# Performance work log

Hardware: AMD Instinct MI355X
Metric: run time of the kernel (lower is better)

The kernel has to match this reference:

```python
import jax, jax.numpy as jnp
import numpy as np

H_HEADS = 4

def setup_inputs() -> dict:
    key = jax.random.key(0)
    ks = jax.random.split(key, 14)
    B, C, H, W = 8, 512, 32, 32
    r = C // H_HEADS  # SE reduction = h per SelfModule(channel, h)
    s_in = 0.02
    inp = {
        'x': jax.random.normal(ks[0], (B, C, H, W), jnp.float32),
        'wq': jax.random.normal(ks[1], (C, C), jnp.float32) * s_in,
        'bq': jnp.zeros((C,), jnp.float32),
        'wk': jax.random.normal(ks[2], (C, C), jnp.float32) * s_in,
        'bk': jnp.zeros((C,), jnp.float32),
        'wv': jax.random.normal(ks[3], (C, C), jnp.float32) * s_in,
        'bv': jnp.zeros((C,), jnp.float32),
        'fc1_w': jax.random.normal(ks[4], (r, C), jnp.float32) * s_in,
        'fc1_b': jnp.zeros((r,), jnp.float32),
        'fc2_w': jax.random.normal(ks[5], (C, r), jnp.float32) * s_in,
        'fc2_b': jnp.zeros((C,), jnp.float32),
        'gate_w': jax.random.normal(ks[6], (1, C), jnp.float32) * s_in,
        'gate_b': jnp.zeros((1,), jnp.float32),
    }
    return inp

def _conv1x1(y, w, b):
    # y: [B,C,H,W], w: [O,C] (1x1 conv kernel squeezed), b: [O]
    return jnp.einsum('bchw,oc->bohw', y, w) + b[None, :, None, None]

def reference(x, wq, bq, wk, bk, wv, bv, fc1_w, fc1_b, fc2_w, fc2_b, gate_w, gate_b):
    B, C, H, W = x.shape
    h = H_HEADS
    dk = C // h
    N = H * W

    # --- SelfScaling (SE without final sigmoid-in-block; sigmoid applied at mul) ---
    p = x.mean(axis=(2, 3))                                   # [B,C] global avg pool
    f = jax.nn.relu(p @ fc1_w.T + fc1_b) @ fc2_w.T + fc2_b    # [B,C]
    x = x * jax.nn.sigmoid(f)[:, :, None, None] + x

    # --- RTrans: conv1x1 QKV, attention over flattened H*W ---
    q = _conv1x1(x, wq, bq).reshape(B, h, dk, N).transpose(0, 1, 3, 2)  # [B,h,N,dk]
    k = _conv1x1(x, wk, bk).reshape(B, h, dk, N)                        # [B,h,dk,N]
    v = _conv1x1(x, wv, bv).reshape(B, h, dk, N)                        # [B,h,dk,N]
    scale = 1.0 / float(np.sqrt(dk))
    att = jax.nn.softmax(jnp.einsum('bhnd,bhdm->bhnm', q, k) * scale, axis=-1)  # [B,h,N,N]
    o = jnp.einsum('bhdn,bhnm->bhdm', v, att).reshape(B, C, H, W)  # v @ att as in torch

    # --- SelfGating ---
    gate = jax.nn.sigmoid(_conv1x1(o, gate_w, gate_b))  # [B,1,H,W]
    return o * gate + o
```

## Files before the change

### kernel.cpp

```cpp
#include <hip/hip_runtime.h>
#include <hip/hip_bf16.h>

#define B_ 8
#define C_ 512
#define N_ 1024
#define HEADS_ 4
#define DK_ 128
#define R_ 128

typedef float f32x4 __attribute__((ext_vector_type(4)));
typedef __bf16 bf16x8 __attribute__((ext_vector_type(8)));
typedef short short4v __attribute__((ext_vector_type(4)));
typedef unsigned short u16;

constexpr float kScale = 0.08838834764831845f;

#define OFF_P   0u
#define OFF_SS  16384u
#define OFF_WB  32768u
#define OFF_XT  1605632u
#define OFF_QT  9994240u
#define OFF_KT  18382848u
#define OFF_V   26771456u
#define OFF_DEN 35160064u
#define OFF_G   35291136u

__device__ __forceinline__ u16 f2b(float f) {
  __hip_bfloat16 h = __float2bfloat16(f);
  return __builtin_bit_cast(u16, h);
}

typedef const __attribute__((address_space(1))) unsigned int* gptr_t;
typedef __attribute__((address_space(3))) unsigned int* lptr_t;
__device__ __forceinline__ void gload16(const void* g, void* l) {
  __builtin_amdgcn_global_load_lds((gptr_t)g, (lptr_t)l, 16, 0, 0);
}

__device__ __forceinline__ f32x4 mfma16(bf16x8 a, bf16x8 b, f32x4 c) {
  return __builtin_amdgcn_mfma_f32_16x16x32_bf16(a, b, c, 0, 0, 0);
}

#if __has_builtin(__builtin_amdgcn_mfma_f32_16x16x16bf16_1k)
__device__ __forceinline__ f32x4 mfma_k16(short4v a, short4v b, f32x4 c) {
  return __builtin_amdgcn_mfma_f32_16x16x16bf16_1k(a, b, c, 0, 0, 0);
}
#else
__device__ __forceinline__ f32x4 mfma_k16(short4v a, short4v b, f32x4 c) {
  bf16x8 a8 = {}, b8 = {};
  for (int e = 0; e < 4; e++) {
    ((u16*)&a8)[e] = ((u16*)&a)[e];
    ((u16*)&b8)[e] = ((u16*)&b)[e];
  }
  return __builtin_amdgcn_mfma_f32_16x16x32_bf16(a8, b8, c, 0, 0, 0);
}
#endif

__global__ __launch_bounds__(64) void k_pool(const float* __restrict__ x,
                                             float* __restrict__ p) {
  int bc = blockIdx.x, lane = threadIdx.x;
  const float4* row = (const float4*)(x + (size_t)bc * N_);
  float s = 0.f;
  for (int i = lane; i < N_ / 4; i += 64) {
    float4 t = row[i];
    s += t.x + t.y + t.z + t.w;
  }
  for (int o = 32; o > 0; o >>= 1) s += __shfl_down(s, o, 64);
  if (lane == 0) p[bc] = s * (1.0f / N_);
}

__global__ __launch_bounds__(256) void k_se(const float* __restrict__ p,
                                            const float* __restrict__ fc1w,
                                            const float* __restrict__ fc1b,
                                            const float* __restrict__ fc2w,
                                            const float* __restrict__ fc2b,
                                            float* __restrict__ ss) {
  __shared__ float pl[C_];
  __shared__ float f1[R_];
  int b = blockIdx.x, t = threadIdx.x;
  for (int c = t; c < C_; c += 256) pl[c] = p[b * C_ + c];
  __syncthreads();
  if (t < R_) {
    float a = fc1b[t];
    for (int c = 0; c < C_; c++) a += pl[c] * fc1w[t * C_ + c];
    f1[t] = fmaxf(a, 0.f);
  }
  __syncthreads();
  for (int c = t; c < C_; c += 256) {
    float a = fc2b[c];
    for (int j = 0; j < R_; j++) a += f1[j] * fc2w[c * R_ + j];
    ss[b * C_ + c] = 1.f + 1.f / (1.f + __expf(-a));
  }
}

__global__ __launch_bounds__(256) void k_castw(const float* __restrict__ wq,
                                               const float* __restrict__ wk,
                                               const float* __restrict__ wv,
                                               u16* __restrict__ wb) {
  int i = blockIdx.x * 256 + threadIdx.x;
  int idx = i * 4;
  const float* srcs[3] = {wq, wk, wv};
  int w = idx / (C_ * C_), off = idx % (C_ * C_);
  float4 v = *(const float4*)(srcs[w] + off);
  u16* d = wb + idx;
  d[0] = f2b(v.x); d[1] = f2b(v.y); d[2] = f2b(v.z); d[3] = f2b(v.w);
}

__global__ __launch_bounds__(256) void k_xt(const float* __restrict__ x,
                                            const float* __restrict__ ss,
                                            u16* __restrict__ xt) {
  int b = blockIdx.z, c0 = blockIdx.y * 64, n0 = blockIdx.x * 64;
  __shared__ float tile[64][65];
  int t = threadIdx.x;
  int cr = t >> 4, nc4 = (t & 15) * 4;
  for (int j = 0; j < 4; j++) {
    int c = cr + j * 16;
    float sc = ss[b * C_ + c0 + c];
    float4 v = *(const float4*)(x + ((size_t)b * C_ + c0 + c) * N_ + n0 + nc4);
    tile[c][nc4 + 0] = v.x * sc;
    tile[c][nc4 + 1] = v.y * sc;
    tile[c][nc4 + 2] = v.z * sc;
    tile[c][nc4 + 3] = v.w * sc;
  }
  __syncthreads();
  int nr = t >> 2, cc = (t & 3) * 16;
  u16 ov[16];
  for (int m = 0; m < 16; m++) ov[m] = f2b(tile[cc + m][nr]);
  u16* dst = xt + ((size_t)b * N_ + n0 + nr) * C_ + c0 + cc;
  for (int m = 0; m < 16; m++) dst[m] = ov[m];
}

__global__ __launch_bounds__(256) void k_qkv(const u16* __restrict__ xt,
                                             const u16* __restrict__ wb,
                                             const float* __restrict__ bq,
                                             const float* __restrict__ bk,
                                             const float* __restrict__ bv,
                                             u16* __restrict__ qt,
                                             u16* __restrict__ kt,
                                             u16* __restrict__ v) {
  __shared__ char smem[32768];
  int b = blockIdx.y / 3, sel = blockIdx.y % 3;
  int tile = blockIdx.x;
  const char *Ab, *Bb;
  u16* out;
  const float* bias;
  int mt, nt, rstride;
  size_t xtoff = (size_t)b * N_ * C_;
  if (sel < 2) {
    mt = tile & 7; nt = tile >> 3;
    Ab = (const char*)(xt + xtoff + (size_t)mt * 128 * C_);
    Bb = (const char*)(wb + (size_t)sel * C_ * C_ + (size_t)nt * 128 * C_);
    out = (sel ? kt : qt) + xtoff;
    bias = sel ? bk : bq;
    rstride = C_ * 2;
  } else {
    mt = tile & 3; nt = tile >> 2;
    Ab = (const char*)(wb + (size_t)2 * C_ * C_ + (size_t)mt * 128 * C_);
    Bb = (const char*)(xt + xtoff + (size_t)nt * 128 * C_);
    out = v + (size_t)b * C_ * N_;
    bias = bv;
    rstride = N_ * 2;
  }
  int t = threadIdx.x, lane = t & 63, wid = t >> 6;
  int wr = wid >> 1, wc = wid & 1;
  const f32x4 z4 = {0.f, 0.f, 0.f, 0.f};
  f32x4 acc[4][4];
  for (int i = 0; i < 4; i++)
    for (int j = 0; j < 4; j++) acc[i][j] = z4;

  char* lA = smem;
  char* lB = smem + 16384;
  for (int ko = 0; ko < C_; ko += 64) {
    __syncthreads();
    for (int i = wid; i < 16; i += 4) {
      int beta = i * 1024 + lane * 16;
      int row = beta >> 7, cb = (beta & 127) ^ ((row & 7) << 4);
      gload16(Ab + (size_t)row * 1024 + ko * 2 + cb, lA + beta);
    }
    for (int i = wid; i < 16; i += 4) {
      int beta = i * 1024 + lane * 16;
      int row = beta >> 7, cb = (beta & 127) ^ ((row & 7) << 4);
      gload16(Bb + (size_t)row * 1024 + ko * 2 + cb, lB + beta);
    }
    __syncthreads();
    for (int ks = 0; ks < 2; ks++) {
      int kb = ks * 64 + (lane >> 4) * 16;
      bf16x8 af[4], bfr[4];
      for (int fi = 0; fi < 4; fi++) {
        int row = wr * 64 + fi * 16 + (lane & 15);
        af[fi] = *(const bf16x8*)(lA + row * 128 + (kb ^ ((row & 7) << 4)));
      }
      for (int fj = 0; fj < 4; fj++) {
        int row = wc * 64 + fj * 16 + (lane & 15);
        bfr[fj] = *(const bf16x8*)(lB + row * 128 + (kb ^ ((row & 7) << 4)));
      }
      for (int fi = 0; fi < 4; fi++)
        for (int fj = 0; fj < 4; fj++)
          acc[fi][fj] = mfma16(af[fi], bfr[fj], acc[fi][fj]);
    }
  }
  __syncthreads();
  for (int fi = 0; fi < 4; fi++)
    for (int fj = 0; fj < 4; fj++) {
      int colb = wc * 64 + fj * 16 + (lane & 15);
      for (int r = 0; r < 4; r++) {
        int rowb = wr * 64 + fi * 16 + (lane >> 4) * 4 + r;
        float bva = (sel < 2) ? bias[nt * 128 + colb] : bias[mt * 128 + rowb];
        float val = acc[fi][fj][r] + bva;
        int byte = rowb * 256 + ((colb * 2) ^ ((rowb & 7) << 4));
        *(u16*)(smem + byte) = f2b(val);
      }
    }
  __syncthreads();
  for (int i = t; i < 2048; i += 256) {
    int row = i >> 4, cb = (i & 15) * 16;
    bf16x8 val = *(const bf16x8*)(smem + row * 256 + (cb ^ ((row & 7) << 4)));
    *(bf16x8*)((char*)out + (size_t)(mt * 128 + row) * rstride + nt * 256 + cb) = val;
  }
}

__global__ __launch_bounds__(256) void k_passA(const u16* __restrict__ qt,
                                               const u16* __restrict__ kt,
                                               float* __restrict__ invden) {
  __shared__ char lK[2][32768];
  int bh = blockIdx.x, nb = blockIdx.y * 128;
  int b = bh >> 2, h = bh & 3;
  const char* qb = (const char*)(qt + (size_t)b * N_ * C_ + h * DK_);
  const char* kb = (const char*)(kt + (size_t)b * N_ * C_ + h * DK_);
  int t = threadIdx.x, lane = t & 63, wid = t >> 6;
  bf16x8 aq[2][4];
  for (int gq = 0; gq < 2; gq++) {
    const char* qr = qb + (size_t)(nb + wid * 32 + gq * 16 + (lane & 15)) * (C_ * 2);
    for (int ks = 0; ks < 4; ks++)
      aq[gq][ks] = *(const bf16x8*)(qr + ks * 64 + (lane >> 4) * 16);
  }
  float sacc[2][4] = {{0.f, 0.f, 0.f, 0.f}, {0.f, 0.f, 0.f, 0.f}};
  const f32x4 z4 = {0.f, 0.f, 0.f, 0.f};
  for (int i = wid; i < 32; i += 4) {
    int beta = i * 1024 + lane * 16;
    int row = beta >> 8, cb = (beta & 255) ^ ((row & 7) << 4);
    gload16(kb + (size_t)row * (C_ * 2) + cb, lK[0] + beta);
  }
  for (int mc = 0; mc < 8; mc++) {
    int cur = mc & 1;
    __syncthreads();
    if (mc < 7) {
      int mnext = (mc + 1) * 128;
      for (int i = wid; i < 32; i += 4) {
        int beta = i * 1024 + lane * 16;
        int row = beta >> 8, cb = (beta & 255) ^ ((row & 7) << 4);
        gload16(kb + (size_t)(mnext + row) * (C_ * 2) + cb, lK[cur ^ 1] + beta);
      }
    }
    for (int fj = 0; fj < 8; fj++) {
      f32x4 s0 = z4, s1 = z4;
      for (int ks = 0; ks < 4; ks++) {
        int row = fj * 16 + (lane & 15);
        bf16x8 bk_ = *(const bf16x8*)(lK[cur] + row * 256 +
                                      ((ks * 64 + (lane >> 4) * 16) ^ ((row & 7) << 4)));
        s0 = mfma16(aq[0][ks], bk_, s0);
        s1 = mfma16(aq[1][ks], bk_, s1);
      }
      for (int r = 0; r < 4; r++) {
        sacc[0][r] += __expf(s0[r] * kScale);
        sacc[1][r] += __expf(s1[r] * kScale);
      }
    }
  }
  for (int gq = 0; gq < 2; gq++)
    for (int r = 0; r < 4; r++) {
      float vv = sacc[gq][r];
      for (int m = 1; m < 16; m <<= 1) vv += __shfl_xor(vv, m, 64);
      sacc[gq][r] = vv;
    }
  if ((lane & 15) == 0) {
    for (int gq = 0; gq < 2; gq++) {
      int n = nb + wid * 32 + gq * 16 + (lane >> 4) * 4;
      for (int r = 0; r < 4; r++) invden[(size_t)bh * N_ + n + r] = 1.f / sacc[gq][r];
    }
  }
}

__global__ __launch_bounds__(256) void k_passB(const u16* __restrict__ qt,
                                               const u16* __restrict__ kt,
                                               const u16* __restrict__ v,
                                               const float* __restrict__ invden,
                                               const float* __restrict__ gw,
                                               float* __restrict__ out,
                                               float* __restrict__ g) {
  __shared__ char lQ[2][16384];
  __shared__ char lV[2][16384];
  __shared__ float gacc[128];
  int bh = blockIdx.x, mb = blockIdx.y * 128;
  int b = bh >> 2, h = bh & 3;
  const char* qb = (const char*)(qt + (size_t)b * N_ * C_ + h * DK_);
  const char* kb = (const char*)(kt + (size_t)b * N_ * C_ + h * DK_);
  const char* vb = (const char*)(v + ((size_t)b * C_ + h * DK_) * N_);
  float* ob = out + ((size_t)b * C_ + h * DK_) * N_ + mb;
  const float* idenb = invden + (size_t)bh * N_;
  int t = threadIdx.x, lane = t & 63, wid = t >> 6;
  bf16x8 bkm[2][4];
  for (int gi = 0; gi < 2; gi++) {
    const char* kr = kb + (size_t)(mb + wid * 32 + gi * 16 + (lane & 15)) * (C_ * 2);
    for (int ks = 0; ks < 4; ks++)
      bkm[gi][ks] = *(const bf16x8*)(kr + ks * 64 + (lane >> 4) * 16);
  }
  if (t < 128) gacc[t] = 0.f;
  const f32x4 z4 = {0.f, 0.f, 0.f, 0.f};
  f32x4 oacc[2][8];
  for (int gi = 0; gi < 2; gi++)
    for (int j = 0; j < 8; j++) oacc[gi][j] = z4;

  for (int i = wid; i < 16; i += 4) {
    int beta = i * 1024 + lane * 16;
    int row = beta >> 8, cb = (beta & 255) ^ ((row & 7) << 4);
    gload16(qb + (size_t)row * (C_ * 2) + cb, lQ[0] + beta);
  }
  for (int i = wid; i < 16; i += 4) {
    int beta = i * 1024 + lane * 16;
    int row = beta >> 7, cb = (beta & 127) ^ ((row & 7) << 4);
    gload16(vb + (size_t)row * (N_ * 2) + cb, lV[0] + beta);
  }

  for (int nc = 0; nc < 16; nc++) {
    int n0 = nc * 64, cur = nc & 1;
    __syncthreads();
    if (nc < 15) {
      int nn = n0 + 64;
      for (int i = wid; i < 16; i += 4) {
        int beta = i * 1024 + lane * 16;
        int row = beta >> 8, cb = (beta & 255) ^ ((row & 7) << 4);
        gload16(qb + (size_t)(nn + row) * (C_ * 2) + cb, lQ[cur ^ 1] + beta);
      }
      for (int i = wid; i < 16; i += 4) {
        int beta = i * 1024 + lane * 16;
        int row = beta >> 7, cb = (beta & 127) ^ ((row & 7) << 4);
        gload16(vb + (size_t)row * (N_ * 2) + nn * 2 + cb, lV[cur ^ 1] + beta);
      }
    }
    short4v pf[2][4];
    for (int fj = 0; fj < 4; fj++) {
      f32x4 s0 = z4, s1 = z4;
      for (int ks = 0; ks < 4; ks++) {
        int row = fj * 16 + (lane & 15);
        bf16x8 aq = *(const bf16x8*)(lQ[cur] + row * 256 +
                                     ((ks * 64 + (lane >> 4) * 16) ^ ((row & 7) << 4)));
        s0 = mfma16(aq, bkm[0][ks], s0);
        s1 = mfma16(aq, bkm[1][ks], s1);
      }
      float4 id4 = *(const float4*)(idenb + n0 + fj * 16 + (lane >> 4) * 4);
      short4v p0, p1;
      p0[0] = (short)f2b(__expf(s0[0] * kScale) * id4.x);
      p0[1] = (short)f2b(__expf(s0[1] * kScale) * id4.y);
      p0[2] = (short)f2b(__expf(s0[2] * kScale) * id4.z);
      p0[3] = (short)f2b(__expf(s0[3] * kScale) * id4.w);
      p1[0] = (short)f2b(__expf(s1[0] * kScale) * id4.x);
      p1[1] = (short)f2b(__expf(s1[1] * kScale) * id4.y);
      p1[2] = (short)f2b(__expf(s1[2] * kScale) * id4.z);
      p1[3] = (short)f2b(__expf(s1[3] * kScale) * id4.w);
      pf[0][fj] = p0;
      pf[1][fj] = p1;
    }
    for (int fd = 0; fd < 8; fd++) {
      int row = fd * 16 + (lane & 15);
      const char* vr = lV[cur] + row * 128;
      int sw = (row & 7) << 4;
      for (int fj = 0; fj < 4; fj++) {
        short4v av = *(const short4v*)(vr + ((fj * 32 + (lane >> 4) * 8) ^ sw));
        oacc[0][fd] = mfma_k16(av, pf[0][fj], oacc[0][fd]);
        oacc[1][fd] = mfma_k16(av, pf[1][fj], oacc[1][fd]);
      }
    }
  }
  __syncthreads();
  for (int gi = 0; gi < 2; gi++) {
    float part = 0.f;
    int mcol = wid * 32 + gi * 16 + (lane & 15);
    for (int fd = 0; fd < 8; fd++) {
      float4 gwv = *(const float4*)(gw + h * DK_ + fd * 16 + (lane >> 4) * 4);
      float gwa[4] = {gwv.x, gwv.y, gwv.z, gwv.w};
      for (int r = 0; r < 4; r++) {
        float val = oacc[gi][fd][r];
        int d = fd * 16 + (lane >> 4) * 4 + r;
        ob[(size_t)d * N_ + mcol] = val;
        part += gwa[r] * val;
      }
    }
    atomicAdd(&gacc[mcol], part);
  }
  __syncthreads();
  if (t < 128) atomicAdd(&g[(size_t)b * N_ + mb + t], gacc[t]);
}

__global__ __launch_bounds__(256) void k_zero_g(float* __restrict__ g) {
  g[blockIdx.x * 256 + threadIdx.x] = 0.f;
}

__global__ __launch_bounds__(256) void k_gate_apply(const float* __restrict__ g,
                                                    const float* __restrict__ gb,
                                                    float* __restrict__ out) {
  size_t i = ((size_t)blockIdx.x * 256 + threadIdx.x) * 4;
  int b = (int)(i / ((size_t)C_ * N_));
  int n = (int)(i & (N_ - 1));
  float4 gv = *(const float4*)(g + (size_t)b * N_ + n);
  float bias = gb[0];
  float4 v = *(float4*)(out + i);
  v.x *= 1.f + 1.f / (1.f + __expf(-(gv.x + bias)));
  v.y *= 1.f + 1.f / (1.f + __expf(-(gv.y + bias)));
  v.z *= 1.f + 1.f / (1.f + __expf(-(gv.z + bias)));
  v.w *= 1.f + 1.f / (1.f + __expf(-(gv.w + bias)));
  *(float4*)(out + i) = v;
}

extern "C" void kernel_launch(void* const* d_in, const int* in_sizes, int n_in,
                              void* d_out, int out_size, void* d_ws, size_t ws_size,
                              hipStream_t stream) {
  const float* x    = (const float*)d_in[0];
  const float* wq   = (const float*)d_in[1];
  const float* bq   = (const float*)d_in[2];
  const float* wk   = (const float*)d_in[3];
  const float* bk   = (const float*)d_in[4];
  const float* wv   = (const float*)d_in[5];
  const float* bv   = (const float*)d_in[6];
  const float* fc1w = (const float*)d_in[7];
  const float* fc1b = (const float*)d_in[8];
  const float* fc2w = (const float*)d_in[9];
  const float* fc2b = (const float*)d_in[10];
  const float* gw   = (const float*)d_in[11];
  const float* gb   = (const float*)d_in[12];
  float* out = (float*)d_out;
  char* ws = (char*)d_ws;

  float* p   = (float*)(ws + OFF_P);
  float* ssc = (float*)(ws + OFF_SS);
  u16* wb  = (u16*)(ws + OFF_WB);
  u16* xt  = (u16*)(ws + OFF_XT);
  u16* qt  = (u16*)(ws + OFF_QT);
  u16* kt  = (u16*)(ws + OFF_KT);
  u16* v   = (u16*)(ws + OFF_V);
  float* den = (float*)(ws + OFF_DEN);
  float* g   = (float*)(ws + OFF_G);

  k_pool<<<B_ * C_, 64, 0, stream>>>(x, p);
  k_castw<<<768, 256, 0, stream>>>(wq, wk, wv, wb);
  k_se<<<B_, 256, 0, stream>>>(p, fc1w, fc1b, fc2w, fc2b, ssc);
  k_zero_g<<<B_ * N_ / 256, 256, 0, stream>>>(g);
  k_xt<<<dim3(16, 8, B_), 256, 0, stream>>>(x, ssc, xt);
  k_qkv<<<dim3(32, B_ * 3), 256, 0, stream>>>(xt, wb, bq, bk, bv, qt, kt, v);
  k_passA<<<dim3(32, 8), 256, 0, stream>>>(qt, kt, den);
  k_passB<<<dim3(32, 8), 256, 0, stream>>>(qt, kt, v, den, gw, out, g);
  k_gate_apply<<<B_ * C_ * N_ / 1024, 256, 0, stream>>>(g, gb, out);
}
```

Before: 127.8 us.

## Split attention passes over key/query halves to double grid parallelism

Pass A now splits the key range into two halves across a new grid dimension and atomically accumulates the softmax denominators, which are zeroed in a merged cast/zero kernel. Pass B splits the query (reduction) dimension into two halves. One half writes to the output and the other to a workspace buffer, and the gate kernel sums the two partial results. This doubles the grid from 256 to 512 blocks so more CUs are used, at the cost of an extra 16MB partial buffer to write and read, atomics, and a per-element reciprocal in pass B. The separate zero kernel launch is also folded into the cast kernel.

```diff
diff --git a/kernel.cpp b/kernel.cpp
--- a/kernel.cpp
+++ b/kernel.cpp
@@ -24,6 +24,7 @@
 #define OFF_V   26771456u
 #define OFF_DEN 35160064u
 #define OFF_G   35291136u
+#define OFF_O1  35323904u
 
 __device__ __forceinline__ u16 f2b(float f) {
   __hip_bfloat16 h = __float2bfloat16(f);
@@ -92,11 +93,22 @@
   }
 }
 
-__global__ __launch_bounds__(256) void k_castw(const float* __restrict__ wq,
-                                               const float* __restrict__ wk,
-                                               const float* __restrict__ wv,
-                                               u16* __restrict__ wb) {
-  int i = blockIdx.x * 256 + threadIdx.x;
+__global__ __launch_bounds__(256) void k_castw_zero(const float* __restrict__ wq,
+                                                    const float* __restrict__ wk,
+                                                    const float* __restrict__ wv,
+                                                    u16* __restrict__ wb,
+                                                    float* __restrict__ g,
+                                                    float* __restrict__ den) {
+  int bid = blockIdx.x;
+  if (bid >= 800) {
+    den[(bid - 800) * 256 + threadIdx.x] = 0.f;
+    return;
+  }
+  if (bid >= 768) {
+    g[(bid - 768) * 256 + threadIdx.x] = 0.f;
+    return;
+  }
+  int i = bid * 256 + threadIdx.x;
   int idx = i * 4;
   const float* srcs[3] = {wq, wk, wv};
   int w = idx / (C_ * C_), off = idx % (C_ * C_);
@@ -220,9 +232,9 @@
 
 __global__ __launch_bounds__(256) void k_passA(const u16* __restrict__ qt,
                                                const u16* __restrict__ kt,
-                                               float* __restrict__ invden) {
+                                               float* __restrict__ den) {
   __shared__ char lK[2][32768];
-  int bh = blockIdx.x, nb = blockIdx.y * 128;
+  int bh = blockIdx.x, nb = blockIdx.y * 128, mh = blockIdx.z;
   int b = bh >> 2, h = bh & 3;
   const char* qb = (const char*)(qt + (size_t)b * N_ * C_ + h * DK_);
   const char* kb = (const char*)(kt + (size_t)b * N_ * C_ + h * DK_);
@@ -235,16 +247,17 @@
   }
   float sacc[2][4] = {{0.f, 0.f, 0.f, 0.f}, {0.f, 0.f, 0.f, 0.f}};
   const f32x4 z4 = {0.f, 0.f, 0.f, 0.f};
+  int m0 = mh * 512;
   for (int i = wid; i < 32; i += 4) {
     int beta = i * 1024 + lane * 16;
     int row = beta >> 8, cb = (beta & 255) ^ ((row & 7) << 4);
-    gload16(kb + (size_t)row * (C_ * 2) + cb, lK[0] + beta);
-  }
-  for (int mc = 0; mc < 8; mc++) {
+    gload16(kb + (size_t)(m0 + row) * (C_ * 2) + cb, lK[0] + beta);
+  }
+  for (int mc = 0; mc < 4; mc++) {
     int cur = mc & 1;
     __syncthreads();
-    if (mc < 7) {
-      int mnext = (mc + 1) * 128;
+    if (mc < 3) {
+      int mnext = m0 + (mc + 1) * 128;
       for (int i = wid; i < 32; i += 4) {
         int beta = i * 1024 + lane * 16;
         int row = beta >> 8, cb = (beta & 255) ^ ((row & 7) << 4);
@@ -275,7 +288,8 @@
   if ((lane & 15) == 0) {
     for (int gq = 0; gq < 2; gq++) {
       int n = nb + wid * 32 + gq * 16 + (lane >> 4) * 4;
-      for (int r = 0; r < 4; r++) invden[(size_t)bh * N_ + n + r] = 1.f / sacc[gq][r];
+      for (int r = 0; r < 4; r++)
+        atomicAdd(&den[(size_t)bh * N_ + n + r], sacc[gq][r]);
     }
   }
 }
@@ -283,20 +297,21 @@
 __global__ __launch_bounds__(256) void k_passB(const u16* __restrict__ qt,
                                                const u16* __restrict__ kt,
                                                const u16* __restrict__ v,
-                                               const float* __restrict__ invden,
+                                               const float* __restrict__ den,
                                                const float* __restrict__ gw,
-                                               float* __restrict__ out,
+                                               float* __restrict__ out0,
+                                               float* __restrict__ o1,
                                                float* __restrict__ g) {
   __shared__ char lQ[2][16384];
   __shared__ char lV[2][16384];
   __shared__ float gacc[128];
-  int bh = blockIdx.x, mb = blockIdx.y * 128;
+  int bh = blockIdx.x, mb = blockIdx.y * 128, nh = blockIdx.z;
   int b = bh >> 2, h = bh & 3;
   const char* qb = (const char*)(qt + (size_t)b * N_ * C_ + h * DK_);
   const char* kb = (const char*)(kt + (size_t)b * N_ * C_ + h * DK_);
   const char* vb = (const char*)(v + ((size_t)b * C_ + h * DK_) * N_);
-  float* ob = out + ((size_t)b * C_ + h * DK_) * N_ + mb;
-  const float* idenb = invden + (size_t)bh * N_;
+  float* ob = (nh ? o1 : out0) + ((size_t)b * C_ + h * DK_) * N_ + mb;
+  const float* denb = den + (size_t)bh * N_;
   int t = threadIdx.x, lane = t & 63, wid = t >> 6;
   bf16x8 bkm[2][4];
   for (int gi = 0; gi < 2; gi++) {
@@ -310,21 +325,22 @@
   for (int gi = 0; gi < 2; gi++)
     for (int j = 0; j < 8; j++) oacc[gi][j] = z4;
 
+  int nbase = nh * 512;
   for (int i = wid; i < 16; i += 4) {
     int beta = i * 1024 + lane * 16;
     int row = beta >> 8, cb = (beta & 255) ^ ((row & 7) << 4);
-    gload16(qb + (size_t)row * (C_ * 2) + cb, lQ[0] + beta);
+    gload16(qb + (size_t)(nbase + row) * (C_ * 2) + cb, lQ[0] + beta);
   }
   for (int i = wid; i < 16; i += 4) {
     int beta = i * 1024 + lane * 16;
     int row = beta >> 7, cb = (beta & 127) ^ ((row & 7) << 4);
-    gload16(vb + (size_t)row * (N_ * 2) + cb, lV[0] + beta);
-  }
-
-  for (int nc = 0; nc < 16; nc++) {
-    int n0 = nc * 64, cur = nc & 1;
+    gload16(vb + (size_t)row * (N_ * 2) + nbase * 2 + cb, lV[0] + beta);
+  }
+
+  for (int c = 0; c < 8; c++) {
+    int n0 = nbase + c * 64, cur = c & 1;
     __syncthreads();
-    if (nc < 15) {
+    if (c < 7) {
       int nn = n0 + 64;
       for (int i = wid; i < 16; i += 4) {
         int beta = i * 1024 + lane * 16;
@@ -347,16 +363,17 @@
         s0 = mfma16(aq, bkm[0][ks], s0);
         s1 = mfma16(aq, bkm[1][ks], s1);
       }
-      float4 id4 = *(const float4*)(idenb + n0 + fj * 16 + (lane >> 4) * 4);
+      float4 d4 = *(const float4*)(denb + (n0 - 0) + fj * 16 + (lane >> 4) * 4);
+      float i0 = 1.f / d4.x, i1 = 1.f / d4.y, i2 = 1.f / d4.z, i3 = 1.f / d4.w;
       short4v p0, p1;
-      p0[0] = (short)f2b(__expf(s0[0] * kScale) * id4.x);
-      p0[1] = (short)f2b(__expf(s0[1] * kScale) * id4.y);
-      p0[2] = (short)f2b(__expf(s0[2] * kScale) * id4.z);
-      p0[3] = (short)f2b(__expf(s0[3] * kScale) * id4.w);
-      p1[0] = (short)f2b(__expf(s1[0] * kScale) * id4.x);
-      p1[1] = (short)f2b(__expf(s1[1] * kScale) * id4.y);
-      p1[2] = (short)f2b(__expf(s1[2] * kScale) * id4.z);
-      p1[3] = (short)f2b(__expf(s1[3] * kScale) * id4.w);
+      p0[0] = (short)f2b(__expf(s0[0] * kScale) * i0);
+      p0[1] = (short)f2b(__expf(s0[1] * kScale) * i1);
+      p0[2] = (short)f2b(__expf(s0[2] * kScale) * i2);
+      p0[3] = (short)f2b(__expf(s0[3] * kScale) * i3);
+      p1[0] = (short)f2b(__expf(s1[0] * kScale) * i0);
+      p1[1] = (short)f2b(__expf(s1[1] * kScale) * i1);
+      p1[2] = (short)f2b(__expf(s1[2] * kScale) * i2);
+      p1[3] = (short)f2b(__expf(s1[3] * kScale) * i3);
       pf[0][fj] = p0;
       pf[1][fj] = p1;
     }
@@ -391,24 +408,24 @@
   if (t < 128) atomicAdd(&g[(size_t)b * N_ + mb + t], gacc[t]);
 }
 
-__global__ __launch_bounds__(256) void k_zero_g(float* __restrict__ g) {
-  g[blockIdx.x * 256 + threadIdx.x] = 0.f;
-}
-
 __global__ __launch_bounds__(256) void k_gate_apply(const float* __restrict__ g,
                                                     const float* __restrict__ gb,
+                                                    const float* __restrict__ o1,
                                                     float* __restrict__ out) {
   size_t i = ((size_t)blockIdx.x * 256 + threadIdx.x) * 4;
   int b = (int)(i / ((size_t)C_ * N_));
   int n = (int)(i & (N_ - 1));
   float4 gv = *(const float4*)(g + (size_t)b * N_ + n);
   float bias = gb[0];
-  float4 v = *(float4*)(out + i);
-  v.x *= 1.f + 1.f / (1.f + __expf(-(gv.x + bias)));
-  v.y *= 1.f + 1.f / (1.f + __expf(-(gv.y + bias)));
-  v.z *= 1.f + 1.f / (1.f + __expf(-(gv.z + bias)));
-  v.w *= 1.f + 1.f / (1.f + __expf(-(gv.w + bias)));
-  *(float4*)(out + i) = v;
+  float4 v0 = *(float4*)(out + i);
+  float4 v1 = *(const float4*)(o1 + i);
+  float ox = v0.x + v1.x, oy = v0.y + v1.y, oz = v0.z + v1.z, ow = v0.w + v1.w;
+  ox *= 1.f + 1.f / (1.f + __expf(-(gv.x + bias)));
+  oy *= 1.f + 1.f / (1.f + __expf(-(gv.y + bias)));
+  oz *= 1.f + 1.f / (1.f + __expf(-(gv.z + bias)));
+  ow *= 1.f + 1.f / (1.f + __expf(-(gv.w + bias)));
+  float4 r = {ox, oy, oz, ow};
+  *(float4*)(out + i) = r;
 }
 
 extern "C" void kernel_launch(void* const* d_in, const int* in_sizes, int n_in,
@@ -439,14 +456,14 @@
   u16* v   = (u16*)(ws + OFF_V);
   float* den = (float*)(ws + OFF_DEN);
   float* g   = (float*)(ws + OFF_G);
+  float* o1  = (float*)(ws + OFF_O1);
 
   k_pool<<<B_ * C_, 64, 0, stream>>>(x, p);
-  k_castw<<<768, 256, 0, stream>>>(wq, wk, wv, wb);
+  k_castw_zero<<<928, 256, 0, stream>>>(wq, wk, wv, wb, g, den);
   k_se<<<B_, 256, 0, stream>>>(p, fc1w, fc1b, fc2w, fc2b, ssc);
-  k_zero_g<<<B_ * N_ / 256, 256, 0, stream>>>(g);
   k_xt<<<dim3(16, 8, B_), 256, 0, stream>>>(x, ssc, xt);
   k_qkv<<<dim3(32, B_ * 3), 256, 0, stream>>>(xt, wb, bq, bk, bv, qt, kt, v);
-  k_passA<<<dim3(32, 8), 256, 0, stream>>>(qt, kt, den);
-  k_passB<<<dim3(32, 8), 256, 0, stream>>>(qt, kt, v, den, gw, out, g);
-  k_gate_apply<<<B_ * C_ * N_ / 1024, 256, 0, stream>>>(g, gb, out);
-}
+  k_passA<<<dim3(32, 8, 2), 256, 0, stream>>>(qt, kt, den);
+  k_passB<<<dim3(32, 8, 2), 256, 0, stream>>>(qt, kt, v, den, gw, out, o1, g);
+  k_gate_apply<<<B_ * C_ * N_ / 1024, 256, 0, stream>>>(g, gb, o1, out);
+}
```

Measured after the change: 123.3 us. 3.6% less time.
